# Kernel tuning notes

Hardware: AMD Instinct MI355X
Metric: run time of the kernel (lower is better)

## Reference

```python
import jax, jax.numpy as jnp
import numpy as np

N = 50000       # nodes
E = 800000      # edges (avg degree 16)
IN_DIM = 256
OUT_DIM = 64
NEG_SLOPE = 0.01  # F.leaky_relu default


def setup_inputs() -> dict:
    key = jax.random.key(0)
    k1, k2, k3, k4, k5 = jax.random.split(key, 5)
    features = jax.random.normal(k1, (N, IN_DIM), dtype=jnp.float32)
    # xavier-normal-ish scaling for weights
    W = jax.random.normal(k2, (IN_DIM, OUT_DIM), dtype=jnp.float32) / np.sqrt(IN_DIM)
    a = jax.random.normal(k3, (2 * OUT_DIM,), dtype=jnp.float32) / np.sqrt(2 * OUT_DIM)
    src = jax.random.randint(k4, (E,), 0, N)
    dst = jax.random.randint(k5, (E,), 0, N)
    return {"features": features, "W": W, "a": a, "src": src, "dst": dst}


def reference(features, W, a, src, dst):
    # z = fc(dropout(features)); dropout p=0 / eval -> identity
    z = features @ W                               # [N, D]
    # attn_fc([z_src || z_dst]) == z_src @ a_l + z_dst @ a_r
    el = z @ a[:OUT_DIM]                           # [N]
    er = z @ a[OUT_DIM:]                           # [N]
    e = jax.nn.leaky_relu(el[src] + er[dst], NEG_SLOPE)  # [E]
    # segment softmax over incoming edges of each destination node
    m = jax.ops.segment_max(e, dst, num_segments=N)      # [N]
    ex = jnp.exp(e - m[dst])                              # [E]
    denom = jax.ops.segment_sum(ex, dst, num_segments=N)  # [N]
    safe_denom = jnp.where(denom == 0, 1.0, denom)
    alpha = ex / safe_denom[dst]                           # [E]
    # weighted aggregation of source features
    h = jax.ops.segment_sum(alpha[:, None] * z[src], dst, num_segments=N)  # [N, D]
    return jax.nn.elu(h)
```

## Files before the change

### kernel.cpp

```cpp
#include <hip/hip_runtime.h>
#include <math.h>
#include <stdint.h>


constexpr int IN_D   = 256;
constexpr int OUT_D  = 64;
constexpr int NBLK   = 256;
constexpr int NBMAX  = 1024;
constexpr int CAPE   = 4096;

typedef _Float16 f16x8 __attribute__((ext_vector_type(8)));
typedef float    f32x4 __attribute__((ext_vector_type(4)));

__device__ __forceinline__ void gload_lds16(const void* g, void* l) {
    __builtin_amdgcn_global_load_lds(
        (const __attribute__((address_space(1))) uint32_t*)g,
        (__attribute__((address_space(3))) uint32_t*)l, 16, 0, 0);
}


__global__ __launch_bounds__(256) void k_count(const int* __restrict__ dst,
                                               int* __restrict__ blkcnt,
                                               int* __restrict__ cursor,
                                               int E, int nb, int chunk) {
    __shared__ int cnt[NBMAX];
    const int b = blockIdx.x, tid = threadIdx.x;
    if (b == 0 && tid == 0) *cursor = 0;
    for (int i = tid; i < nb; i += 256) cnt[i] = 0;
    __syncthreads();
    const int lo = b * chunk;
    const int hi = (lo + chunk < E) ? lo + chunk : E;
    const int nv = (hi - lo) & ~3;
    for (int e = lo + tid * 4; e < lo + nv; e += 1024) {
        int4 d4 = *(const int4*)&dst[e];
        atomicAdd(&cnt[d4.x >> 6], 1);
        atomicAdd(&cnt[d4.y >> 6], 1);
        atomicAdd(&cnt[d4.z >> 6], 1);
        atomicAdd(&cnt[d4.w >> 6], 1);
    }
    for (int e = lo + nv + tid; e < hi; e += 256) atomicAdd(&cnt[dst[e] >> 6], 1);
    __syncthreads();
    for (int i = tid; i < nb; i += 256) blkcnt[(size_t)b * NBMAX + i] = cnt[i];
}

__global__ __launch_bounds__(256) void k_bsum(int* __restrict__ blkcnt,
                                              int* __restrict__ total,
                                              int* __restrict__ bbase,
                                              int* __restrict__ cursor, int nb) {
    const int j = blockIdx.x * 256 + threadIdx.x;
    const int lane = threadIdx.x & 63;
    int run = 0;
    if (j < nb) {
        #pragma unroll 8
        for (int b = 0; b < NBLK; ++b) {
            int v = blkcnt[(size_t)b * NBMAX + j];
            blkcnt[(size_t)b * NBMAX + j] = run;
            run += v;
        }
    }
    const int runp = (run + 3) & ~3;
    int incl = runp;
    #pragma unroll
    for (int ofs = 1; ofs < 64; ofs <<= 1) {
        int u = __shfl_up(incl, ofs, 64);
        if (lane >= ofs) incl += u;
    }
    int base = 0;
    if (lane == 63) base = atomicAdd(cursor, incl);
    base = __shfl(base, 63, 64);
    if (j < nb) { total[j] = run; bbase[j] = base + incl - runp; }
}

__global__ __launch_bounds__(256) void k_bin(const int* __restrict__ dst,
                                             const int* __restrict__ src,
                                             const int* __restrict__ blkcnt,
                                             const int* __restrict__ bbase,
                                             uint32_t* __restrict__ binned,
                                             int E, int nb, int chunk) {
    __shared__ int cur[NBMAX];
    const int b = blockIdx.x, tid = threadIdx.x;
    for (int i = tid; i < nb; i += 256)
        cur[i] = bbase[i] + blkcnt[(size_t)b * NBMAX + i];
    __syncthreads();
    const int lo = b * chunk;
    const int hi = (lo + chunk < E) ? lo + chunk : E;
    const int nv = (hi - lo) & ~3;
    for (int e = lo + tid * 4; e < lo + nv; e += 1024) {
        int4 d4 = *(const int4*)&dst[e];
        int4 s4 = *(const int4*)&src[e];
        int p;
        p = atomicAdd(&cur[d4.x >> 6], 1); binned[p] = ((uint32_t)d4.x << 16) | (uint32_t)s4.x;
        p = atomicAdd(&cur[d4.y >> 6], 1); binned[p] = ((uint32_t)d4.y << 16) | (uint32_t)s4.y;
        p = atomicAdd(&cur[d4.z >> 6], 1); binned[p] = ((uint32_t)d4.z << 16) | (uint32_t)s4.z;
        p = atomicAdd(&cur[d4.w >> 6], 1); binned[p] = ((uint32_t)d4.w << 16) | (uint32_t)s4.w;
    }
    for (int e = lo + nv + tid; e < hi; e += 256) {
        const uint32_t d = (uint32_t)dst[e];
        const int pos = atomicAdd(&cur[d >> 6], 1);
        binned[pos] = (d << 16) | (uint32_t)src[e];
    }
}


__global__ void k_wconv(const float* __restrict__ W, _Float16* __restrict__ Wf) {
    int t = blockIdx.x * 256 + threadIdx.x;
    int j    = t & 7;
    int lane = (t >> 3) & 63;
    int ct   = (t >> 9) & 3;
    int kc   = t >> 11;
    int k = kc * 32 + (lane >> 4) * 8 + j;
    int c = ct * 16 + (lane & 15);
    Wf[t] = (_Float16)W[k * OUT_D + c];
}

__global__ __launch_bounds__(256) void k_gemmf16(
        const float* __restrict__ feat, const _Float16* __restrict__ Wf,
        const float* __restrict__ a,
        _Float16* __restrict__ z, float* __restrict__ el, float* __restrict__ er,
        int n)
{
    __shared__ __align__(16) _Float16 WfL[IN_D * OUT_D];

    const int tid  = threadIdx.x;
    const int lane = tid & 63;
    const int wv   = tid >> 6;
    const int row0 = blockIdx.x * 64 + wv * 16;
    const int kg   = lane >> 4;

    int gr = row0 + (lane & 15); if (gr > n - 1) gr = n - 1;
    const float* frow = feat + (size_t)gr * IN_D;
    float4 r0[8], r1[8];
    #pragma unroll
    for (int kc = 0; kc < 8; ++kc) {
        const float4* fp = (const float4*)(frow + kc * 32 + kg * 8);
        r0[kc] = fp[0];
        r1[kc] = fp[1];
    }

    #pragma unroll
    for (int i = 0; i < 8; ++i) {
        const char* gsrc = (const char*)Wf + (size_t)(i * 256 + tid) * 16;
        char* ldst = (char*)WfL + (size_t)(i * 256 + wv * 64) * 16;
        gload_lds16(gsrc, ldst);
    }
    __syncthreads();

    f32x4 acc[4];
    #pragma unroll
    for (int ct = 0; ct < 4; ++ct) acc[ct] = (f32x4){0.f, 0.f, 0.f, 0.f};

    #pragma unroll
    for (int kc = 0; kc < 8; ++kc) {
        f16x8 af;
        af[0] = (_Float16)r0[kc].x; af[1] = (_Float16)r0[kc].y;
        af[2] = (_Float16)r0[kc].z; af[3] = (_Float16)r0[kc].w;
        af[4] = (_Float16)r1[kc].x; af[5] = (_Float16)r1[kc].y;
        af[6] = (_Float16)r1[kc].z; af[7] = (_Float16)r1[kc].w;
        #pragma unroll
        for (int ct = 0; ct < 4; ++ct) {
            f16x8 bf = *(const f16x8*)&WfL[((kc * 4 + ct) * 64 + lane) * 8];
            acc[ct] = __builtin_amdgcn_mfma_f32_16x16x32_f16(af, bf, acc[ct], 0, 0, 0);
        }
    }

    const int col = lane & 15;
    float av[4], bv[4];
    #pragma unroll
    for (int ct = 0; ct < 4; ++ct) {
        av[ct] = a[ct * 16 + col];
        bv[ct] = a[OUT_D + ct * 16 + col];
    }
    #pragma unroll
    for (int i = 0; i < 4; ++i) {
        const int r = row0 + (lane >> 4) * 4 + i;
        float vl = 0.f, vr = 0.f;
        #pragma unroll
        for (int ct = 0; ct < 4; ++ct) {
            float zv = acc[ct][i];
            if (r < n) z[(size_t)r * OUT_D + ct * 16 + col] = (_Float16)zv;
            vl = fmaf(zv, av[ct], vl);
            vr = fmaf(zv, bv[ct], vr);
        }
        #pragma unroll
        for (int msk = 8; msk >= 1; msk >>= 1) {
            vl += __shfl_xor(vl, msk, 64);
            vr += __shfl_xor(vr, msk, 64);
        }
        if (col == 0 && r < n) { el[r] = vl; er[r] = vr; }
    }
}

__global__ __launch_bounds__(1024) void k_fagg(
        const uint32_t* __restrict__ binned, const int* __restrict__ bbase,
        const int* __restrict__ total,
        const _Float16* __restrict__ z, const float* __restrict__ el,
        const float* __restrict__ er, float* __restrict__ out, int n)
{
    __shared__ __align__(16) uint32_t pr[CAPE];
    __shared__ uint16_t adjs[CAPE];
    __shared__ int fcnt[64], foff[64], fcur[64];

    const int j   = blockIdx.x, tid = threadIdx.x;
    const int lane = tid & 63;
    const int wv   = tid >> 6;
    const int ebase = bbase[j];
    int ecnt = total[j]; if (ecnt > CAPE) ecnt = CAPE;

    const int nv4 = (ecnt + 3) >> 2;
    for (int i = tid; i < nv4; i += 1024)
        *(uint4*)&pr[i * 4] = *(const uint4*)&binned[ebase + i * 4];
    if (tid < 64) { fcnt[tid] = 0; fcur[tid] = 0; }
    __syncthreads();
    for (int i = tid; i < ecnt; i += 1024)
        atomicAdd(&fcnt[(pr[i] >> 16) & 63], 1);
    __syncthreads();
    if (tid < 64) {
        const int v = fcnt[tid];
        int incl = v;
        #pragma unroll
        for (int ofs = 1; ofs < 64; ofs <<= 1) {
            int u = __shfl_up(incl, ofs, 64);
            if (tid >= ofs) incl += u;
        }
        foff[tid] = incl - v;
    }
    __syncthreads();
    for (int i = tid; i < ecnt; i += 1024) {
        const uint32_t u = pr[i];
        const int ld = (u >> 16) & 63;
        const int r = atomicAdd(&fcur[ld], 1);
        adjs[foff[ld] + r] = (uint16_t)(u & 0xFFFFu);
    }
    __syncthreads();

    const int g     = lane >> 4;
    const int qc    = lane & 15;
    const int gbase = lane & 48;

    const int ld  = wv * 4 + g;
    const int d   = j * 64 + ld;
    const bool ok = (d < n);
    const int deg = ok ? fcnt[ld] : 0;
    const int sb  = ok ? foff[ld] : 0;
    const float erd = ok ? er[d] : 0.f;

    float m = -INFINITY, den = 0.f;
    float4 acc = {0.f, 0.f, 0.f, 0.f};
    for (int c0 = 0; c0 < deg; c0 += 16) {
        const int i = c0 + qc;
        int s = 0;
        float lgv = -INFINITY;
        if (i < deg) {
            s = adjs[sb + i];
            const float x = el[s] + erd;
            lgv = x > 0.f ? x : 0.01f * x;
        }
        float cm = lgv;
        #pragma unroll
        for (int msk = 8; msk >= 1; msk >>= 1) cm = fmaxf(cm, __shfl_xor(cm, msk, 16));
        const float newm = fmaxf(m, cm);
        const float ex = (i < deg) ? __expf(lgv - newm) : 0.f;
        float sum = ex;
        #pragma unroll
        for (int msk = 8; msk >= 1; msk >>= 1) sum += __shfl_xor(sum, msk, 16);
        const float scale = __expf(m - newm);
        den = den * scale + sum;
        acc.x *= scale; acc.y *= scale; acc.z *= scale; acc.w *= scale;
        m = newm;

        const int cd = (deg - c0 < 16) ? deg - c0 : 16;
        for (int q = 0; q < cd; ++q) {
            const float wq = __shfl(ex, gbase + q, 64);
            const int   sq = __shfl(s,  gbase + q, 64);
            uint2 v = *(const uint2*)&z[(size_t)sq * OUT_D + qc * 4];
            const _Float16* hf = (const _Float16*)&v;
            acc.x = fmaf(wq, (float)hf[0], acc.x);
            acc.y = fmaf(wq, (float)hf[1], acc.y);
            acc.z = fmaf(wq, (float)hf[2], acc.z);
            acc.w = fmaf(wq, (float)hf[3], acc.w);
        }
    }
    if (ok) {
        const float inv = (deg > 0) ? 1.f / den : 0.f;
        float4 h;
        h.x = acc.x * inv; h.y = acc.y * inv; h.z = acc.z * inv; h.w = acc.w * inv;
        h.x = h.x > 0.f ? h.x : expm1f(h.x);
        h.y = h.y > 0.f ? h.y : expm1f(h.y);
        h.z = h.z > 0.f ? h.z : expm1f(h.z);
        h.w = h.w > 0.f ? h.w : expm1f(h.w);
        *(float4*)&out[(size_t)d * OUT_D + qc * 4] = h;
    }
}

extern "C" void kernel_launch(void* const* d_in, const int* in_sizes, int n_in,
                              void* d_out, int out_size, void* d_ws, size_t ws_size,
                              hipStream_t stream) {
    const float* feat = (const float*)d_in[0];
    const float* W    = (const float*)d_in[1];
    const float* a    = (const float*)d_in[2];
    const int*   src  = (const int*)d_in[3];
    const int*   dst  = (const int*)d_in[4];
    const int n = in_sizes[0] / IN_D;
    const int E = in_sizes[3];
    float* out = (float*)d_out;

    const int nb = (n + 63) >> 6;
    const int chunk = (((E + NBLK - 1) / NBLK) + 3) & ~3;

    char* ws = (char*)d_ws;
    _Float16* z_h = (_Float16*)ws;    ws += (size_t)n * OUT_D * 2;
    float* el = (float*)ws;           ws += (size_t)n * 4;
    float* er = (float*)ws;           ws += (size_t)n * 4;
    int*  total = (int*)ws;           ws += (size_t)NBMAX * 4;
    int*  bbase = (int*)ws;           ws += (size_t)NBMAX * 4;
    int*  cursor = (int*)ws;          ws += 16;
    int*  blkcnt = (int*)ws;          ws += (size_t)NBLK * NBMAX * 4;
    uint32_t* binned = (uint32_t*)ws; ws += ((size_t)E + 4 * NBMAX) * 4;
    _Float16* Wf = (_Float16*)ws;

    k_count<<<NBLK, 256, 0, stream>>>(dst, blkcnt, cursor, E, nb, chunk);
    k_bsum<<<(nb + 255) / 256, 256, 0, stream>>>(blkcnt, total, bbase, cursor, nb);
    k_bin<<<NBLK, 256, 0, stream>>>(dst, src, blkcnt, bbase, binned, E, nb, chunk);
    k_wconv<<<IN_D * OUT_D / 256, 256, 0, stream>>>(W, Wf);
    k_gemmf16<<<(n + 63) / 64, 256, 0, stream>>>(feat, Wf, a, z_h, el, er, n);
    k_fagg<<<nb, 1024, 0, stream>>>(binned, bbase, total, z_h, el, er, out, n);
}
```

Measured before the change: 154.8 us.

## Fuse weight conversion into GEMM, replace atomic bin base with scan, unroll gather

Removes the separate W-to-fp16 conversion kernel: each GEMM block now reads fp32 W and converts it while writing into its swizzled LDS layout. The bin base offsets now come from a dedicated single-block scan kernel instead of a cross-wave atomic cursor, which also drops the cursor reset. The aggregation gather loop is unrolled by four, padding the edge count up to a multiple of four. The tradeoffs are an extra launch for the scan, each of ~782 GEMM blocks redoing the conversion, and possible reads past the valid edges in the padded gather.

Result: no change. 152.7 us (-1.4%).

```diff
diff --git a/kernel.cpp b/kernel.cpp
--- a/kernel.cpp
+++ b/kernel.cpp
@@ -12,20 +12,12 @@
 typedef _Float16 f16x8 __attribute__((ext_vector_type(8)));
 typedef float    f32x4 __attribute__((ext_vector_type(4)));
 
-__device__ __forceinline__ void gload_lds16(const void* g, void* l) {
-    __builtin_amdgcn_global_load_lds(
-        (const __attribute__((address_space(1))) uint32_t*)g,
-        (__attribute__((address_space(3))) uint32_t*)l, 16, 0, 0);
-}
-
 
 __global__ __launch_bounds__(256) void k_count(const int* __restrict__ dst,
                                                int* __restrict__ blkcnt,
-                                               int* __restrict__ cursor,
                                                int E, int nb, int chunk) {
     __shared__ int cnt[NBMAX];
     const int b = blockIdx.x, tid = threadIdx.x;
-    if (b == 0 && tid == 0) *cursor = 0;
     for (int i = tid; i < nb; i += 256) cnt[i] = 0;
     __syncthreads();
     const int lo = b * chunk;
@@ -44,31 +36,35 @@
 }
 
 __global__ __launch_bounds__(256) void k_bsum(int* __restrict__ blkcnt,
-                                              int* __restrict__ total,
-                                              int* __restrict__ bbase,
-                                              int* __restrict__ cursor, int nb) {
+                                              int* __restrict__ total, int nb) {
     const int j = blockIdx.x * 256 + threadIdx.x;
-    const int lane = threadIdx.x & 63;
+    if (j >= nb) return;
     int run = 0;
-    if (j < nb) {
-        #pragma unroll 8
-        for (int b = 0; b < NBLK; ++b) {
-            int v = blkcnt[(size_t)b * NBMAX + j];
-            blkcnt[(size_t)b * NBMAX + j] = run;
-            run += v;
-        }
-    }
-    const int runp = (run + 3) & ~3;
-    int incl = runp;
-    #pragma unroll
-    for (int ofs = 1; ofs < 64; ofs <<= 1) {
-        int u = __shfl_up(incl, ofs, 64);
-        if (lane >= ofs) incl += u;
-    }
-    int base = 0;
-    if (lane == 63) base = atomicAdd(cursor, incl);
-    base = __shfl(base, 63, 64);
-    if (j < nb) { total[j] = run; bbase[j] = base + incl - runp; }
+    #pragma unroll 8
+    for (int b = 0; b < NBLK; ++b) {
+        int v = blkcnt[(size_t)b * NBMAX + j];
+        blkcnt[(size_t)b * NBMAX + j] = run;
+        run += v;
+    }
+    total[j] = run;
+}
+
+__global__ __launch_bounds__(1024) void k_scan1(const int* __restrict__ total,
+                                                int* __restrict__ bbase, int nb) {
+    __shared__ int sh[1024];
+    const int t = threadIdx.x;
+    const int v = (t < nb) ? ((total[t] + 3) & ~3) : 0;
+    sh[t] = v;
+    __syncthreads();
+    int acc = v;
+    for (int ofs = 1; ofs < 1024; ofs <<= 1) {
+        int u = (t >= ofs) ? sh[t - ofs] : 0;
+        __syncthreads();
+        acc += u;
+        sh[t] = acc;
+        __syncthreads();
+    }
+    if (t < nb) bbase[t] = acc - v;
 }
 
 __global__ __launch_bounds__(256) void k_bin(const int* __restrict__ dst,
@@ -102,19 +98,8 @@
 }
 
 
-__global__ void k_wconv(const float* __restrict__ W, _Float16* __restrict__ Wf) {
-    int t = blockIdx.x * 256 + threadIdx.x;
-    int j    = t & 7;
-    int lane = (t >> 3) & 63;
-    int ct   = (t >> 9) & 3;
-    int kc   = t >> 11;
-    int k = kc * 32 + (lane >> 4) * 8 + j;
-    int c = ct * 16 + (lane & 15);
-    Wf[t] = (_Float16)W[k * OUT_D + c];
-}
-
 __global__ __launch_bounds__(256) void k_gemmf16(
-        const float* __restrict__ feat, const _Float16* __restrict__ Wf,
+        const float* __restrict__ feat, const float* __restrict__ W,
         const float* __restrict__ a,
         _Float16* __restrict__ z, float* __restrict__ el, float* __restrict__ er,
         int n)
@@ -138,10 +123,19 @@
     }
 
     #pragma unroll
-    for (int i = 0; i < 8; ++i) {
-        const char* gsrc = (const char*)Wf + (size_t)(i * 256 + tid) * 16;
-        char* ldst = (char*)WfL + (size_t)(i * 256 + wv * 64) * 16;
-        gload_lds16(gsrc, ldst);
+    for (int r = 0; r < 16; ++r) {
+        const int i4 = r * 256 + tid;
+        float4 w4 = ((const float4*)W)[i4];
+        const int k  = i4 >> 4;
+        const int c0 = (i4 & 15) * 4;
+        const int kc = k >> 5, kr = k & 31;
+        const int j  = kr & 7, lhi = kr >> 3;
+        const int ct = c0 >> 4;
+        const int t0 = ((kc * 4 + ct) * 64 + lhi * 16 + (c0 & 15)) * 8 + j;
+        WfL[t0]      = (_Float16)w4.x;
+        WfL[t0 + 8]  = (_Float16)w4.y;
+        WfL[t0 + 16] = (_Float16)w4.z;
+        WfL[t0 + 24] = (_Float16)w4.w;
     }
     __syncthreads();
 
@@ -268,16 +262,20 @@
         acc.x *= scale; acc.y *= scale; acc.z *= scale; acc.w *= scale;
         m = newm;
 
-        const int cd = (deg - c0 < 16) ? deg - c0 : 16;
-        for (int q = 0; q < cd; ++q) {
-            const float wq = __shfl(ex, gbase + q, 64);
-            const int   sq = __shfl(s,  gbase + q, 64);
-            uint2 v = *(const uint2*)&z[(size_t)sq * OUT_D + qc * 4];
-            const _Float16* hf = (const _Float16*)&v;
-            acc.x = fmaf(wq, (float)hf[0], acc.x);
-            acc.y = fmaf(wq, (float)hf[1], acc.y);
-            acc.z = fmaf(wq, (float)hf[2], acc.z);
-            acc.w = fmaf(wq, (float)hf[3], acc.w);
+        const int cd  = (deg - c0 < 16) ? deg - c0 : 16;
+        const int cd4 = (cd + 3) & ~3;
+        for (int q = 0; q < cd4; q += 4) {
+            #pragma unroll
+            for (int u = 0; u < 4; ++u) {
+                const float wq = __shfl(ex, gbase + q + u, 64);
+                const int   sq = __shfl(s,  gbase + q + u, 64);
+                uint2 v = *(const uint2*)&z[(size_t)sq * OUT_D + qc * 4];
+                const _Float16* hf = (const _Float16*)&v;
+                acc.x = fmaf(wq, (float)hf[0], acc.x);
+                acc.y = fmaf(wq, (float)hf[1], acc.y);
+                acc.z = fmaf(wq, (float)hf[2], acc.z);
+                acc.w = fmaf(wq, (float)hf[3], acc.w);
+            }
         }
     }
     if (ok) {
@@ -313,15 +311,13 @@
     float* er = (float*)ws;           ws += (size_t)n * 4;
     int*  total = (int*)ws;           ws += (size_t)NBMAX * 4;
     int*  bbase = (int*)ws;           ws += (size_t)NBMAX * 4;
-    int*  cursor = (int*)ws;          ws += 16;
     int*  blkcnt = (int*)ws;          ws += (size_t)NBLK * NBMAX * 4;
-    uint32_t* binned = (uint32_t*)ws; ws += ((size_t)E + 4 * NBMAX) * 4;
-    _Float16* Wf = (_Float16*)ws;
-
-    k_count<<<NBLK, 256, 0, stream>>>(dst, blkcnt, cursor, E, nb, chunk);
-    k_bsum<<<(nb + 255) / 256, 256, 0, stream>>>(blkcnt, total, bbase, cursor, nb);
+    uint32_t* binned = (uint32_t*)ws;
+
+    k_count<<<NBLK, 256, 0, stream>>>(dst, blkcnt, E, nb, chunk);
+    k_bsum<<<(nb + 255) / 256, 256, 0, stream>>>(blkcnt, total, nb);
+    k_scan1<<<1, 1024, 0, stream>>>(total, bbase, nb);
     k_bin<<<NBLK, 256, 0, stream>>>(dst, src, blkcnt, bbase, binned, E, nb, chunk);
-    k_wconv<<<IN_D * OUT_D / 256, 256, 0, stream>>>(W, Wf);
-    k_gemmf16<<<(n + 63) / 64, 256, 0, stream>>>(feat, Wf, a, z_h, el, er, n);
+    k_gemmf16<<<(n + 63) / 64, 256, 0, stream>>>(feat, W, a, z_h, el, er, n);
     k_fagg<<<nb, 1024, 0, stream>>>(binned, bbase, total, z_h, el, er, out, n);
 }
```
